# Kernel optimization log

Measured on AMD Instinct MI355X. Metric: run time of the kernel, lower is better.

Reference implementation:

```python
import jax, jax.numpy as jnp
import numpy as np

NUM_GRAPHS = 512


def gcn_layer(x, W, b, row, col, ew):
    # x: [N, Fin] -> [N, Fout]; row/col/ew: [E+N] (self-loops appended)
    N = x.shape[0]
    xw = x @ W                                        # [N, Fout]
    deg = jax.ops.segment_sum(ew, row, num_segments=N)
    dinv = jnp.where(deg > 0, jax.lax.rsqrt(deg), 0.0)  # deg^-1/2, inf->0
    norm = dinv[row] * ew * dinv[col]                 # [E+N]
    msg = norm[:, None] * xw[col]                     # gather + scale
    out = jax.ops.segment_sum(msg, row, num_segments=N)
    return out + b


def build_graph(edge_index, N, dtype):
    # remove_self_loops equivalent: zero-weight self-loop edges (same deg & aggregation)
    src, dst = edge_index[0], edge_index[1]
    ew = (src != dst).astype(dtype)                   # [E]
    loops = jnp.arange(N, dtype=edge_index.dtype)
    row = jnp.concatenate([src, loops])
    col = jnp.concatenate([dst, loops])
    ew = jnp.concatenate([ew, jnp.ones((N,), dtype)])  # loop_weight = 1 (improved=False)
    return row, col, ew


def setup_inputs() -> dict:
    key = jax.random.key(0)
    ks = jax.random.split(key, 8)
    N, E, F = 100000, 1600000, 64
    x = jax.random.normal(ks[0], (N, F), dtype=jnp.float32)
    edge_index = jax.random.randint(ks[1], (2, E), 0, N, dtype=jnp.int64)
    batch = jnp.sort(jax.random.randint(ks[2], (N,), 0, NUM_GRAPHS, dtype=jnp.int64))
    s = 1.0 / np.sqrt(F)
    W1 = jax.random.normal(ks[3], (F, F), dtype=jnp.float32) * s
    W2 = jax.random.normal(ks[4], (F, F), dtype=jnp.float32) * s
    W3 = jax.random.normal(ks[5], (F, F), dtype=jnp.float32) * s
    b1 = jnp.zeros((F,), jnp.float32)
    b2 = jnp.zeros((F,), jnp.float32)
    b3 = jnp.zeros((F,), jnp.float32)
    return {"x": x, "edge_index": edge_index, "batch": batch,
            "W1": W1, "b1": b1, "W2": W2, "b2": b2, "W3": W3, "b3": b3}


def reference(x, edge_index, batch, W1, b1, W2, b2, W3, b3):
    N = x.shape[0]
    row, col, ew = build_graph(edge_index, N, x.dtype)
    h = gcn_layer(x, W1, b1, row, col, ew)
    h = jax.nn.relu(h)                                # dropout p=0 / eval: identity
    h = gcn_layer(h, W2, b2, row, col, ew)
    h = jax.nn.relu(h)
    h = gcn_layer(h, W3, b3, row, col, ew)
    # global_add_pool over graph ids
    return jax.ops.segment_sum(h, batch, num_segments=NUM_GRAPHS)  # [G, F]
```

## Files before the change

kernel.cpp:

```cpp
#include <hip/hip_runtime.h>
#include <hip/hip_fp16.h>

#define F 64
#define SLOTS 48
#define NPART 8
#define WG_PER_PART 512

typedef __attribute__((ext_vector_type(8))) _Float16 f16x8;
typedef __attribute__((ext_vector_type(4))) float    f32x4;

__global__ __launch_bounds__(256) void build_csr(
        const int* __restrict__ src, const int* __restrict__ dst,
        int* __restrict__ cnt, int* __restrict__ col, int E, int N, int psize) {
    int w = blockIdx.x;
    int p = w & (NPART - 1);
    int c = w >> 3;
    int lo = p * psize, hi = min(N, lo + psize);
    int chunk = (E + WG_PER_PART - 1) / WG_PER_PART;
    int ebeg = c * chunk, eend = min(E, ebeg + chunk);
    for (int e = ebeg + threadIdx.x; e < eend; e += 256) {
        int s = __builtin_nontemporal_load(src + e);
        int d = __builtin_nontemporal_load(dst + e);
        if (s >= lo && s < hi && s != d) {
            int pos = atomicAdd(&cnt[s], 1);
            if (pos < SLOTS) col[(size_t)s * SLOTS + pos] = d;
        }
    }
}

__global__ void compute_dinv(const int* __restrict__ cnt, float* __restrict__ dinv, int N) {
    int i = blockIdx.x * blockDim.x + threadIdx.x;
    if (i >= N) return;
    int deg = min(cnt[i], SLOTS) + 1;
    dinv[i] = rsqrtf((float)deg);
}

__global__ void prep_w(const float* __restrict__ W1, const float* __restrict__ W2,
                       const float* __restrict__ W3, __half* __restrict__ Wf) {
    const float* W = (blockIdx.x == 0) ? W1 : (blockIdx.x == 1) ? W2 : W3;
    __half* out = Wf + (size_t)blockIdx.x * 4096;
    int t = threadIdx.x;
    #pragma unroll
    for (int rep = 0; rep < 2; ++rep) {
        int tri = t + rep * 256;
        int ct = tri >> 7;
        int kb = (tri >> 6) & 1;
        int l  = tri & 63;
        #pragma unroll
        for (int j = 0; j < 8; ++j) {
            int k  = kb * 32 + (l >> 4) * 8 + j;
            int cc = ct * 16 + (l & 15);
            out[(size_t)((ct * 2 + kb) * 64 + l) * 8 + j] = __float2half(W[k * F + cc]);
        }
    }
}

template <bool FP32IN>
__global__ __launch_bounds__(256) void gemm_mfma(
        const void* __restrict__ xin, const __half* __restrict__ Wf,
        const float* __restrict__ dinv, __half* __restrict__ y, int N) {
    int wave = threadIdx.x >> 6, lane = threadIdx.x & 63;
    int rowbase = blockIdx.x * 128 + wave * 32;
    if (rowbase >= N) return;
    int a = lane >> 4;
    int r15 = lane & 15;

    f16x8 bf[4][2];
    #pragma unroll
    for (int ct = 0; ct < 4; ++ct)
        #pragma unroll
        for (int kb = 0; kb < 2; ++kb)
            bf[ct][kb] = *(const f16x8*)(Wf + (size_t)((ct * 2 + kb) * 64 + lane) * 8);

    f16x8 af[2][2];
    #pragma unroll
    for (int rt = 0; rt < 2; ++rt) {
        int row = rowbase + rt * 16 + r15;
        if (row > N - 1) row = N - 1;
        #pragma unroll
        for (int kb = 0; kb < 2; ++kb) {
            if (FP32IN) {
                const float* xr = (const float*)xin + (size_t)row * F + kb * 32 + a * 8;
                float4 v0 = *(const float4*)xr;
                float4 v1 = *(const float4*)(xr + 4);
                union { f16x8 v; __half2 h2[4]; } u;
                u.h2[0] = __floats2half2_rn(v0.x, v0.y);
                u.h2[1] = __floats2half2_rn(v0.z, v0.w);
                u.h2[2] = __floats2half2_rn(v1.x, v1.y);
                u.h2[3] = __floats2half2_rn(v1.z, v1.w);
                af[rt][kb] = u.v;
            } else {
                const __half* xr = (const __half*)xin + (size_t)row * F + kb * 32 + a * 8;
                af[rt][kb] = *(const f16x8*)xr;
            }
        }
    }

    f32x4 acc[2][4];
    #pragma unroll
    for (int rt = 0; rt < 2; ++rt)
        #pragma unroll
        for (int ct = 0; ct < 4; ++ct)
            acc[rt][ct] = (f32x4){0.f, 0.f, 0.f, 0.f};

    #pragma unroll
    for (int rt = 0; rt < 2; ++rt)
        #pragma unroll
        for (int ct = 0; ct < 4; ++ct)
            #pragma unroll
            for (int kb = 0; kb < 2; ++kb)
                acc[rt][ct] = __builtin_amdgcn_mfma_f32_16x16x32_f16(
                    af[rt][kb], bf[ct][kb], acc[rt][ct], 0, 0, 0);

    #pragma unroll
    for (int rt = 0; rt < 2; ++rt) {
        #pragma unroll
        for (int r = 0; r < 4; ++r) {
            int row = rowbase + rt * 16 + a * 4 + r;
            if (row < N) {
                float dv = dinv[row];
                #pragma unroll
                for (int ct = 0; ct < 4; ++ct)
                    y[(size_t)row * F + ct * 16 + r15] = __float2half(dv * acc[rt][ct][r]);
            }
        }
    }
}

__global__ __launch_bounds__(256) void aggregate(
        const __half* __restrict__ y, const int* __restrict__ cnt,
        const int* __restrict__ col, const float* __restrict__ dinv,
        const float* __restrict__ b, __half* __restrict__ out, int N, int do_relu) {
    int wid = (int)((blockIdx.x * blockDim.x + threadIdx.x) >> 6);
    int lane = threadIdx.x & 63;
    if (wid >= N) return;
    int deg = min(cnt[wid], SLOTS);
    int slot = lane >> 5;
    int f2 = lane & 31;

    int cl = 0;
    if (lane < deg) cl = col[(size_t)wid * SLOTS + lane];

    const __half2* yb = (const __half2*)y;
    float ax = 0.f, ay = 0.f;

    if (slot == 0) {
        float2 v = __half22float2(yb[(size_t)wid * 32 + f2]);
        ax += v.x; ay += v.y;
    }

    int e = 0;
    for (; e + 8 <= deg; e += 8) {
        int i0 = __shfl(cl, e + 0 + slot, 64);
        int i1 = __shfl(cl, e + 2 + slot, 64);
        int i2 = __shfl(cl, e + 4 + slot, 64);
        int i3 = __shfl(cl, e + 6 + slot, 64);
        float2 v0 = __half22float2(yb[(size_t)i0 * 32 + f2]);
        float2 v1 = __half22float2(yb[(size_t)i1 * 32 + f2]);
        float2 v2 = __half22float2(yb[(size_t)i2 * 32 + f2]);
        float2 v3 = __half22float2(yb[(size_t)i3 * 32 + f2]);
        ax += v0.x; ay += v0.y;
        ax += v1.x; ay += v1.y;
        ax += v2.x; ay += v2.y;
        ax += v3.x; ay += v3.y;
    }
    for (; e + 4 <= deg; e += 4) {
        int i0 = __shfl(cl, e + 0 + slot, 64);
        int i1 = __shfl(cl, e + 2 + slot, 64);
        float2 v0 = __half22float2(yb[(size_t)i0 * 32 + f2]);
        float2 v1 = __half22float2(yb[(size_t)i1 * 32 + f2]);
        ax += v0.x; ay += v0.y;
        ax += v1.x; ay += v1.y;
    }
    for (; e < deg; e += 2) {
        int idx = e + slot;
        int i0 = __shfl(cl, min(idx, deg - 1), 64);
        float2 v = __half22float2(yb[(size_t)i0 * 32 + f2]);
        if (idx < deg) { ax += v.x; ay += v.y; }
    }

    ax += __shfl_xor(ax, 32, 64);
    ay += __shfl_xor(ay, 32, 64);

    if (slot == 0) {
        float dv = dinv[wid];
        float2 bb = ((const float2*)b)[f2];
        float vx = fmaf(dv, ax, bb.x);
        float vy = fmaf(dv, ay, bb.y);
        if (do_relu) { vx = fmaxf(vx, 0.f); vy = fmaxf(vy, 0.f); }
        ((__half2*)out)[(size_t)wid * 32 + f2] = __floats2half2_rn(vx, vy);
    }
}

__global__ __launch_bounds__(256) void pool_kernel(
        const __half* __restrict__ h, const int* __restrict__ batch,
        float* __restrict__ out, int N) {
    __shared__ float red[4][16][4];
    int g = blockIdx.x;
    int tid = threadIdx.x;
    int w = tid >> 6, lane = tid & 63;
    int f4 = lane & 15;
    int rs = (tid >> 4);

    int lo = 0, hi = N;
    while (lo < hi) { int m = (lo + hi) >> 1; if (batch[m] < g) lo = m + 1; else hi = m; }
    int lo2 = lo, hi2 = N;
    while (lo2 < hi2) { int m = (lo2 + hi2) >> 1; if (batch[m] < g + 1) lo2 = m + 1; else hi2 = m; }

    const uint2* hb = (const uint2*)h;
    float a0 = 0.f, a1 = 0.f, a2 = 0.f, a3 = 0.f;
    for (int i = lo + rs; i < lo2; i += 16) {
        uint2 v = hb[(size_t)i * 16 + f4];
        float2 f0 = __half22float2(*(const __half2*)&v.x);
        float2 f1 = __half22float2(*(const __half2*)&v.y);
        a0 += f0.x; a1 += f0.y; a2 += f1.x; a3 += f1.y;
    }
    a0 += __shfl_xor(a0, 16, 64); a1 += __shfl_xor(a1, 16, 64);
    a2 += __shfl_xor(a2, 16, 64); a3 += __shfl_xor(a3, 16, 64);
    a0 += __shfl_xor(a0, 32, 64); a1 += __shfl_xor(a1, 32, 64);
    a2 += __shfl_xor(a2, 32, 64); a3 += __shfl_xor(a3, 32, 64);
    if (lane < 16) {
        red[w][f4][0] = a0; red[w][f4][1] = a1;
        red[w][f4][2] = a2; red[w][f4][3] = a3;
    }
    __syncthreads();
    if (w == 0 && lane < 16) {
        float4 o;
        o.x = red[0][f4][0] + red[1][f4][0] + red[2][f4][0] + red[3][f4][0];
        o.y = red[0][f4][1] + red[1][f4][1] + red[2][f4][1] + red[3][f4][1];
        o.z = red[0][f4][2] + red[1][f4][2] + red[2][f4][2] + red[3][f4][2];
        o.w = red[0][f4][3] + red[1][f4][3] + red[2][f4][3] + red[3][f4][3];
        *(float4*)(out + (size_t)g * F + f4 * 4) = o;
    }
}

extern "C" void kernel_launch(void* const* d_in, const int* in_sizes, int n_in,
                              void* d_out, int out_size, void* d_ws, size_t ws_size,
                              hipStream_t stream) {
    const float* x    = (const float*)d_in[0];
    const int*   eidx = (const int*)d_in[1];
    const int*   batch = (const int*)d_in[2];
    const float* W1 = (const float*)d_in[3];
    const float* b1 = (const float*)d_in[4];
    const float* W2 = (const float*)d_in[5];
    const float* b2 = (const float*)d_in[6];
    const float* W3 = (const float*)d_in[7];
    const float* b3 = (const float*)d_in[8];

    int N = in_sizes[0] / F;
    int E = in_sizes[1] / 2;
    int G = out_size / F;
    const int* src = eidx;
    const int* dst = eidx + E;

    char* ws = (char*)d_ws;
    size_t off = 0;
    auto alloc = [&](size_t bytes) -> void* {
        void* p = ws + off;
        off = (off + bytes + 255) & ~(size_t)255;
        return p;
    };
    __half* y    = (__half*)alloc((size_t)N * F * 2);
    __half* h    = (__half*)alloc((size_t)N * F * 2);
    int*    col  = (int*)alloc((size_t)N * SLOTS * 4);
    int*    cnt  = (int*)alloc((size_t)N * 4);
    float*  dinv = (float*)alloc((size_t)N * 4);
    __half* Wf   = (__half*)alloc(3 * 4096 * 2);
    (void)ws_size; (void)n_in;

    int psize = (N + NPART - 1) / NPART;

    hipMemsetAsync(cnt, 0, (size_t)N * 4, stream);
    build_csr<<<NPART * WG_PER_PART, 256, 0, stream>>>(src, dst, cnt, col, E, N, psize);
    compute_dinv<<<(N + 255) / 256, 256, 0, stream>>>(cnt, dinv, N);
    prep_w<<<3, 256, 0, stream>>>(W1, W2, W3, Wf);

    int gemm_grid = (N + 127) / 128;
    int agg_grid  = (int)(((size_t)N * 64 + 255) / 256);

    gemm_mfma<true><<<gemm_grid, 256, 0, stream>>>(x, Wf, dinv, y, N);
    aggregate<<<agg_grid, 256, 0, stream>>>(y, cnt, col, dinv, b1, h, N, 1);
    gemm_mfma<false><<<gemm_grid, 256, 0, stream>>>(h, Wf + 4096, dinv, y, N);
    aggregate<<<agg_grid, 256, 0, stream>>>(y, cnt, col, dinv, b2, h, N, 1);
    gemm_mfma<false><<<gemm_grid, 256, 0, stream>>>(h, Wf + 8192, dinv, y, N);
    aggregate<<<agg_grid, 256, 0, stream>>>(y, cnt, col, dinv, b3, h, N, 0);

    pool_kernel<<<G, 256, 0, stream>>>(h, batch, (float*)d_out, N);
}
```

Before: 334.6 us.

## Fuse aggregation with following layer GEMM via shared-memory tile

Adds a fused kernel in which each wave aggregates 32 nodes into LDS, applies bias and ReLU, then runs the next layer's MFMA GEMM on that tile. This removes the intermediate h write and reread between aggregate and GEMM for layers 1 and 2, and drops two launches. The trade-off is much less parallelism: one wave now handles 32 nodes sequentially instead of one wave per node, which may hide gather latency poorly. The CSR build is also changed to load dst only for edges whose source falls in the partition, and it drops the nontemporal loads.

```diff
diff --git a/kernel.cpp b/kernel.cpp
--- a/kernel.cpp
+++ b/kernel.cpp
@@ -19,11 +19,13 @@
     int chunk = (E + WG_PER_PART - 1) / WG_PER_PART;
     int ebeg = c * chunk, eend = min(E, ebeg + chunk);
     for (int e = ebeg + threadIdx.x; e < eend; e += 256) {
-        int s = __builtin_nontemporal_load(src + e);
-        int d = __builtin_nontemporal_load(dst + e);
-        if (s >= lo && s < hi && s != d) {
-            int pos = atomicAdd(&cnt[s], 1);
-            if (pos < SLOTS) col[(size_t)s * SLOTS + pos] = d;
+        int s = src[e];
+        if (s >= lo && s < hi) {
+            int d = dst[e];
+            if (s != d) {
+                int pos = atomicAdd(&cnt[s], 1);
+                if (pos < SLOTS) col[(size_t)s * SLOTS + pos] = d;
+            }
         }
     }
 }
@@ -127,6 +129,118 @@
     }
 }
 
+__global__ __launch_bounds__(256) void fused_agg_gemm(
+        const __half* __restrict__ y, const int* __restrict__ cnt,
+        const int* __restrict__ col, const float* __restrict__ dinv,
+        const float* __restrict__ bias, const __half* __restrict__ Wf,
+        __half* __restrict__ yout, int N) {
+    __shared__ __half hbuf[4][32][72];
+    int wave = threadIdx.x >> 6, lane = threadIdx.x & 63;
+    int nodebase = blockIdx.x * 128 + wave * 32;
+    int slot = lane >> 5;
+    int f2 = lane & 31;
+    const __half2* yb = (const __half2*)y;
+
+    for (int t = 0; t < 32; ++t) {
+        int n = nodebase + t;
+        if (n > N - 1) n = N - 1;
+        int deg = min(cnt[n], SLOTS);
+        int cl = 0;
+        if (lane < deg) cl = col[(size_t)n * SLOTS + lane];
+
+        float ax = 0.f, ay = 0.f;
+        if (slot == 0) {
+            float2 v = __half22float2(yb[(size_t)n * 32 + f2]);
+            ax += v.x; ay += v.y;
+        }
+        int e = 0;
+        for (; e + 8 <= deg; e += 8) {
+            int i0 = __shfl(cl, e + 0 + slot, 64);
+            int i1 = __shfl(cl, e + 2 + slot, 64);
+            int i2 = __shfl(cl, e + 4 + slot, 64);
+            int i3 = __shfl(cl, e + 6 + slot, 64);
+            float2 v0 = __half22float2(yb[(size_t)i0 * 32 + f2]);
+            float2 v1 = __half22float2(yb[(size_t)i1 * 32 + f2]);
+            float2 v2 = __half22float2(yb[(size_t)i2 * 32 + f2]);
+            float2 v3 = __half22float2(yb[(size_t)i3 * 32 + f2]);
+            ax += v0.x; ay += v0.y;
+            ax += v1.x; ay += v1.y;
+            ax += v2.x; ay += v2.y;
+            ax += v3.x; ay += v3.y;
+        }
+        for (; e + 4 <= deg; e += 4) {
+            int i0 = __shfl(cl, e + 0 + slot, 64);
+            int i1 = __shfl(cl, e + 2 + slot, 64);
+            float2 v0 = __half22float2(yb[(size_t)i0 * 32 + f2]);
+            float2 v1 = __half22float2(yb[(size_t)i1 * 32 + f2]);
+            ax += v0.x; ay += v0.y;
+            ax += v1.x; ay += v1.y;
+        }
+        for (; e < deg; e += 2) {
+            int idx = e + slot;
+            int i0 = __shfl(cl, min(idx, deg - 1), 64);
+            float2 v = __half22float2(yb[(size_t)i0 * 32 + f2]);
+            if (idx < deg) { ax += v.x; ay += v.y; }
+        }
+        ax += __shfl_xor(ax, 32, 64);
+        ay += __shfl_xor(ay, 32, 64);
+        if (slot == 0) {
+            float dv = dinv[n];
+            float2 bb = ((const float2*)bias)[f2];
+            float vx = fmaxf(fmaf(dv, ax, bb.x), 0.f);
+            float vy = fmaxf(fmaf(dv, ay, bb.y), 0.f);
+            *(__half2*)&hbuf[wave][t][2 * f2] = __floats2half2_rn(vx, vy);
+        }
+    }
+    __syncthreads();
+
+    int a = lane >> 4;
+    int r15 = lane & 15;
+    f16x8 bf[4][2];
+    #pragma unroll
+    for (int ct = 0; ct < 4; ++ct)
+        #pragma unroll
+        for (int kb = 0; kb < 2; ++kb)
+            bf[ct][kb] = *(const f16x8*)(Wf + (size_t)((ct * 2 + kb) * 64 + lane) * 8);
+
+    f16x8 af[2][2];
+    #pragma unroll
+    for (int rt = 0; rt < 2; ++rt)
+        #pragma unroll
+        for (int kb = 0; kb < 2; ++kb)
+            af[rt][kb] = *(const f16x8*)&hbuf[wave][rt * 16 + r15][kb * 32 + a * 8];
+
+    f32x4 acc[2][4];
+    #pragma unroll
+    for (int rt = 0; rt < 2; ++rt)
+        #pragma unroll
+        for (int ct = 0; ct < 4; ++ct)
+            acc[rt][ct] = (f32x4){0.f, 0.f, 0.f, 0.f};
+
+    #pragma unroll
+    for (int rt = 0; rt < 2; ++rt)
+        #pragma unroll
+        for (int ct = 0; ct < 4; ++ct)
+            #pragma unroll
+            for (int kb = 0; kb < 2; ++kb)
+                acc[rt][ct] = __builtin_amdgcn_mfma_f32_16x16x32_f16(
+                    af[rt][kb], bf[ct][kb], acc[rt][ct], 0, 0, 0);
+
+    #pragma unroll
+    for (int rt = 0; rt < 2; ++rt) {
+        #pragma unroll
+        for (int r = 0; r < 4; ++r) {
+            int row = nodebase + rt * 16 + a * 4 + r;
+            if (row < N) {
+                float dv = dinv[row];
+                #pragma unroll
+                for (int ct = 0; ct < 4; ++ct)
+                    yout[(size_t)row * F + ct * 16 + r15] = __float2half(dv * acc[rt][ct][r]);
+            }
+        }
+    }
+}
+
 __global__ __launch_bounds__(256) void aggregate(
         const __half* __restrict__ y, const int* __restrict__ cnt,
         const int* __restrict__ col, const float* __restrict__ dinv,
@@ -143,12 +257,10 @@
 
     const __half2* yb = (const __half2*)y;
     float ax = 0.f, ay = 0.f;
-
     if (slot == 0) {
         float2 v = __half22float2(yb[(size_t)wid * 32 + f2]);
         ax += v.x; ay += v.y;
     }
-
     int e = 0;
     for (; e + 8 <= deg; e += 8) {
         int i0 = __shfl(cl, e + 0 + slot, 64);
@@ -178,10 +290,8 @@
         float2 v = __half22float2(yb[(size_t)i0 * 32 + f2]);
         if (idx < deg) { ax += v.x; ay += v.y; }
     }
-
     ax += __shfl_xor(ax, 32, 64);
     ay += __shfl_xor(ay, 32, 64);
-
     if (slot == 0) {
         float dv = dinv[wid];
         float2 bb = ((const float2*)b)[f2];
@@ -275,15 +385,12 @@
     compute_dinv<<<(N + 255) / 256, 256, 0, stream>>>(cnt, dinv, N);
     prep_w<<<3, 256, 0, stream>>>(W1, W2, W3, Wf);
 
-    int gemm_grid = (N + 127) / 128;
+    int tile_grid = (N + 127) / 128;
     int agg_grid  = (int)(((size_t)N * 64 + 255) / 256);
 
-    gemm_mfma<true><<<gemm_grid, 256, 0, stream>>>(x, Wf, dinv, y, N);
-    aggregate<<<agg_grid, 256, 0, stream>>>(y, cnt, col, dinv, b1, h, N, 1);
-    gemm_mfma<false><<<gemm_grid, 256, 0, stream>>>(h, Wf + 4096, dinv, y, N);
-    aggregate<<<agg_grid, 256, 0, stream>>>(y, cnt, col, dinv, b2, h, N, 1);
-    gemm_mfma<false><<<gemm_grid, 256, 0, stream>>>(h, Wf + 8192, dinv, y, N);
+    gemm_mfma<true><<<tile_grid, 256, 0, stream>>>(x, Wf, dinv, y, N);
+    fused_agg_gemm<<<tile_grid, 256, 0, stream>>>(y, cnt, col, dinv, b1, Wf + 4096, h, N);
+    fused_agg_gemm<<<tile_grid, 256, 0, stream>>>(h, cnt, col, dinv, b2, Wf + 8192, y, N);
     aggregate<<<agg_grid, 256, 0, stream>>>(y, cnt, col, dinv, b3, h, N, 0);
-
     pool_kernel<<<G, 256, 0, stream>>>(h, batch, (float*)d_out, N);
 }
```

Result: slower. 382.0 us (+14.2%).
